# Kernel tuning notes

Hardware: AMD Instinct MI355X
Metric: run time of the kernel (lower is better)

Reference implementation:

```python
import jax, jax.numpy as jnp
import numpy as np
import math

B, S, H = 2, 2048, 1024
NH = 16
HD = H // NH  # 64


def setup_inputs() -> dict:
    key = jax.random.key(0)
    ks = jax.random.split(key, 4)
    scale = 1.0 / math.sqrt(H)
    return {
        "hidden_states": jax.random.normal(ks[0], (B, S, H), dtype=jnp.float32),
        "attention_mask": jnp.ones((B, S), dtype=jnp.float32),
        "Wq": jax.random.normal(ks[1], (H, H), dtype=jnp.float32) * scale,
        "bq": jnp.zeros((H,), dtype=jnp.float32),
        "Wk": jax.random.normal(ks[2], (H, H), dtype=jnp.float32) * scale,
        "bk": jnp.zeros((H,), dtype=jnp.float32),
        "Wv": jax.random.normal(ks[3], (H, H), dtype=jnp.float32) * scale,
        "bv": jnp.zeros((H,), dtype=jnp.float32),
    }


def _split_heads(x):
    # [B, S, H] -> [B, NH, S, HD]
    b, s, _ = x.shape
    return x.reshape(b, s, NH, HD).transpose(0, 2, 1, 3)


def reference(hidden_states, attention_mask, Wq, bq, Wk, bk, Wv, bv):
    q = _split_heads(hidden_states @ Wq.T + bq)  # [B, NH, S, HD]
    k = _split_heads(hidden_states @ Wk.T + bk)
    v = _split_heads(hidden_states @ Wv.T + bv)

    # [B, NH, S, S] attention scores
    scores = jnp.einsum("bhqd,bhkd->bhqk", q, k) / math.sqrt(HD)
    # mask: [B, S] -> additive bias [B, 1, 1, S]
    bias = (1.0 - attention_mask)[:, None, None, :] * -10000.0
    probs = jax.nn.softmax(scores + bias, axis=-1)
    # dropout prob = 0.0 (eval semantics) -> identity

    ctx = jnp.einsum("bhqk,bhkd->bhqd", probs, v)  # [B, NH, S, HD]
    ctx = ctx.transpose(0, 2, 1, 3).reshape(hidden_states.shape[0], hidden_states.shape[1], H)
    return ctx
```

## Files before the change

kernel.cpp:

```cpp
#include <hip/hip_runtime.h>
#include <hip/hip_bf16.h>

typedef __bf16 bf16;
typedef __bf16 bf16x4 __attribute__((ext_vector_type(4)));
typedef __bf16 bf16x8 __attribute__((ext_vector_type(8)));
typedef float f32x4 __attribute__((ext_vector_type(4)));

#define GLP(p) ((const __attribute__((address_space(1))) void*)(p))
#define LDSP(p) ((__attribute__((address_space(3))) void*)(p))

__global__ __launch_bounds__(256) void cvt_kernel(const float* __restrict__ in,
                                                  bf16* __restrict__ out, int n4) {
  int i = blockIdx.x * 256 + threadIdx.x;
  if (i < n4) {
    float4 v = reinterpret_cast<const float4*>(in)[i];
    bf16x4 o = { (bf16)v.x, (bf16)v.y, (bf16)v.z, (bf16)v.w };
    reinterpret_cast<bf16x4*>(out)[i] = o;
  }
}

__global__ __launch_bounds__(256) void qkv_gemm(
    const bf16* __restrict__ Xb, const bf16* __restrict__ Wb,
    const float* __restrict__ biasq, const float* __restrict__ biask,
    const float* __restrict__ biasv,
    bf16* __restrict__ Qb, bf16* __restrict__ Kb, bf16* __restrict__ Vt) {
  __shared__ __align__(16) bf16 As[128 * 32];
  __shared__ __align__(16) bf16 Bs[128 * 32];
  const int tid = threadIdx.x;
  const int w = tid >> 6, l = tid & 63;
  const int lg = l >> 4, lr = l & 15;
  const int wr = w >> 1, wc = w & 1;
  const int bm = blockIdx.y * 128, bn = blockIdx.x * 128;

  f32x4 acc[4][4] = {};

  #pragma unroll 1
  for (int k0 = 0; k0 < 1024; k0 += 32) {
    #pragma unroll
    for (int i = 0; i < 2; ++i) {
      int row = i * 64 + (tid >> 2);
      int c8 = (tid & 3) * 8;
      __builtin_amdgcn_global_load_lds(GLP(Xb + (bm + row) * 1024 + k0 + c8),
                                       LDSP((char*)As + (i * 256 + w * 64) * 16),
                                       16, 0, 0);
      __builtin_amdgcn_global_load_lds(GLP(Wb + (bn + row) * 1024 + k0 + c8),
                                       LDSP((char*)Bs + (i * 256 + w * 64) * 16),
                                       16, 0, 0);
    }
    __syncthreads();
    bf16x8 af[4], bfq[4];
    #pragma unroll
    for (int t = 0; t < 4; ++t) {
      af[t]  = *reinterpret_cast<const bf16x8*>(
                   reinterpret_cast<const char*>(As) + (wr * 64 + t * 16 + lr) * 64 + lg * 16);
      bfq[t] = *reinterpret_cast<const bf16x8*>(
                   reinterpret_cast<const char*>(Bs) + (wc * 64 + t * 16 + lr) * 64 + lg * 16);
    }
    #pragma unroll
    for (int mt = 0; mt < 4; ++mt)
      #pragma unroll
      for (int nt = 0; nt < 4; ++nt)
        acc[mt][nt] = __builtin_amdgcn_mfma_f32_16x16x32_bf16(af[mt], bfq[nt], acc[mt][nt], 0, 0, 0);
    __syncthreads();
  }

  const int mtx = blockIdx.x >> 3;
  const float* bp = (mtx == 0) ? biasq : (mtx == 1) ? biask : biasv;
  #pragma unroll
  for (int nt = 0; nt < 4; ++nt) {
    int ng = bn + wc * 64 + nt * 16 + lr;
    int nj = ng & 1023;
    int hh = nj >> 6, d = nj & 63;
    float bias = bp[nj];
    #pragma unroll
    for (int mt = 0; mt < 4; ++mt) {
      int m0 = bm + wr * 64 + mt * 16 + lg * 4;
      int bb = m0 >> 11, s0 = m0 & 2047;
      if (mtx == 2) {
        bf16x4 pk;
        #pragma unroll
        for (int r = 0; r < 4; ++r) pk[r] = (bf16)(acc[mt][nt][r] + bias);
        *reinterpret_cast<bf16x4*>(Vt + (((bb * 16 + hh) * 64 + d) * 2048 + s0)) = pk;
      } else {
        bf16* dst = (mtx == 0) ? Qb : Kb;
        #pragma unroll
        for (int r = 0; r < 4; ++r)
          dst[((bb * 16 + hh) * 2048 + s0 + r) * 64 + d] = (bf16)(acc[mt][nt][r] + bias);
      }
    }
  }
}

__global__ __launch_bounds__(256) void attn_kernel(
    const bf16* __restrict__ Qb, const bf16* __restrict__ Kb,
    const bf16* __restrict__ Vt, const float* __restrict__ mask,
    float* __restrict__ out) {
  __shared__ __align__(16) bf16 Ks[64 * 64];
  __shared__ __align__(16) bf16 Vs[64 * 64];
  __shared__ __align__(16) bf16 Pl[4][16 * 72];
  const int tid = threadIdx.x;
  const int w = tid >> 6, l = tid & 63;
  const int lg = l >> 4, lr = l & 15;
  const int blk = blockIdx.x;
  const int xcd = blk & 7, i0 = blk >> 3;
  const int bh = xcd * 4 + (i0 >> 5), qt = i0 & 31;
  const int bb = bh >> 4, hh = bh & 15;
  const int q16 = qt * 64 + w * 16;

  const bf16* Qp = Qb + (bh * 2048 + q16) * 64;
  const bf16* Kp = Kb + bh * 2048 * 64;
  const bf16* Vp = Vt + bh * 64 * 2048;
  const float* mp = mask + bb * 2048;

  bf16x8 aq[2];
  #pragma unroll
  for (int kk = 0; kk < 2; ++kk)
    aq[kk] = *reinterpret_cast<const bf16x8*>(Qp + lr * 64 + kk * 32 + lg * 8);

  f32x4 acc[4] = {};
  float mrun = -3.0e38f;
  float lrun = 0.f;

  const float SC = 0.125f * 1.44269504f;
  const float MB = -10000.0f * 1.44269504f;
  bf16* pw = &Pl[w][0];
  const int srow = tid >> 3, sch = tid & 7;

  #pragma unroll 1
  for (int kv0 = 0; kv0 < 2048; kv0 += 64) {
    #pragma unroll
    for (int p = 0; p < 2; ++p) {
      int rw = p * 32 + srow;
      int chg = sch ^ (rw & 7);
      __builtin_amdgcn_global_load_lds(GLP(Kp + (kv0 + rw) * 64 + chg * 8),
                                       LDSP((char*)Ks + (p * 256 + w * 64) * 16), 16, 0, 0);
      __builtin_amdgcn_global_load_lds(GLP(Vp + rw * 2048 + kv0 + chg * 8),
                                       LDSP((char*)Vs + (p * 256 + w * 64) * 16), 16, 0, 0);
    }
    __syncthreads();

    f32x4 sa[4];
    #pragma unroll
    for (int t = 0; t < 4; ++t) {
      f32x4 z = {};
      #pragma unroll
      for (int kk = 0; kk < 2; ++kk) {
        bf16x8 bk8 = *reinterpret_cast<const bf16x8*>(
            reinterpret_cast<const char*>(Ks) + (t * 16 + lr) * 128 + ((kk * 4 + lg) ^ (lr & 7)) * 16);
        z = __builtin_amdgcn_mfma_f32_16x16x32_bf16(bk8, aq[kk], z, 0, 0, 0);
      }
      sa[t] = z;
    }
    #pragma unroll
    for (int t = 0; t < 4; ++t) {
      float4 mk = *reinterpret_cast<const float4*>(mp + kv0 + t * 16 + lg * 4);
      sa[t][0] = sa[t][0] * SC + (1.0f - mk.x) * MB;
      sa[t][1] = sa[t][1] * SC + (1.0f - mk.y) * MB;
      sa[t][2] = sa[t][2] * SC + (1.0f - mk.z) * MB;
      sa[t][3] = sa[t][3] * SC + (1.0f - mk.w) * MB;
    }
    float rm = sa[0][0];
    #pragma unroll
    for (int t = 0; t < 4; ++t)
      #pragma unroll
      for (int r = 0; r < 4; ++r) rm = fmaxf(rm, sa[t][r]);
    rm = fmaxf(rm, __shfl_xor(rm, 16));
    rm = fmaxf(rm, __shfl_xor(rm, 32));
    float mn = fmaxf(mrun, rm);
    float fac = exp2f(mrun - mn);
    mrun = mn;
    float rs = 0.f;
    #pragma unroll
    for (int t = 0; t < 4; ++t)
      #pragma unroll
      for (int r = 0; r < 4; ++r) {
        float p = exp2f(sa[t][r] - mn);
        sa[t][r] = p;
        rs += p;
      }
    rs += __shfl_xor(rs, 16);
    rs += __shfl_xor(rs, 32);
    lrun = lrun * fac + rs;
    float facq[4];
    #pragma unroll
    for (int r = 0; r < 4; ++r) facq[r] = __shfl(fac, ((l >> 4) << 2) + r);
    #pragma unroll
    for (int nt = 0; nt < 4; ++nt)
      #pragma unroll
      for (int r = 0; r < 4; ++r) acc[nt][r] *= facq[r];
    #pragma unroll
    for (int t = 0; t < 4; ++t) {
      bf16x4 pk = { (bf16)sa[t][0], (bf16)sa[t][1], (bf16)sa[t][2], (bf16)sa[t][3] };
      *reinterpret_cast<bf16x4*>(pw + lr * 72 + t * 16 + lg * 4) = pk;
    }
    asm volatile("" ::: "memory");
    #pragma unroll
    for (int ks = 0; ks < 2; ++ks) {
      bf16x8 pa = *reinterpret_cast<const bf16x8*>(
          reinterpret_cast<const char*>(pw) + lr * 144 + ks * 64 + lg * 16);
      #pragma unroll
      for (int nt = 0; nt < 4; ++nt) {
        bf16x8 bv8 = *reinterpret_cast<const bf16x8*>(
            reinterpret_cast<const char*>(Vs) + (nt * 16 + lr) * 128 + ((ks * 4 + lg) ^ (lr & 7)) * 16);
        acc[nt] = __builtin_amdgcn_mfma_f32_16x16x32_bf16(pa, bv8, acc[nt], 0, 0, 0);
      }
    }
    __syncthreads();
  }

  #pragma unroll
  for (int r = 0; r < 4; ++r) {
    float lq = __shfl(lrun, ((l >> 4) << 2) + r);
    float inv = 1.0f / lq;
    int sq = q16 + lg * 4 + r;
    #pragma unroll
    for (int nt = 0; nt < 4; ++nt) {
      int d = nt * 16 + lr;
      out[((bb * 2048 + sq) * 16 + hh) * 64 + d] = acc[nt][r] * inv;
    }
  }
}

extern "C" void kernel_launch(void* const* d_in, const int* in_sizes, int n_in,
                              void* d_out, int out_size, void* d_ws, size_t ws_size,
                              hipStream_t stream) {
  const float* hs   = (const float*)d_in[0];
  const float* mask = (const float*)d_in[1];
  const float* Wq   = (const float*)d_in[2];
  const float* bq   = (const float*)d_in[3];
  const float* Wk   = (const float*)d_in[4];
  const float* bk   = (const float*)d_in[5];
  const float* Wv   = (const float*)d_in[6];
  const float* bv   = (const float*)d_in[7];
  float* out = (float*)d_out;

  if (ws_size < 39845888u) return;
  bf16* Xb = (bf16*)d_ws;
  bf16* Wb = Xb + 4194304;
  bf16* Qb = Wb + 3145728;
  bf16* Kb = Qb + 4194304;
  bf16* Vt = Kb + 4194304;

  cvt_kernel<<<4096, 256, 0, stream>>>(hs, Xb, 1048576);
  cvt_kernel<<<1024, 256, 0, stream>>>(Wq, Wb, 262144);
  cvt_kernel<<<1024, 256, 0, stream>>>(Wk, Wb + 1048576, 262144);
  cvt_kernel<<<1024, 256, 0, stream>>>(Wv, Wb + 2097152, 262144);
  qkv_gemm<<<dim3(24, 32), 256, 0, stream>>>(Xb, Wb, bq, bk, bv, Qb, Kb, Vt);
  attn_kernel<<<1024, 256, 0, stream>>>(Qb, Kb, Vt, mask, out);
}
```

Before: 219.8 us.

## Fuse conversions, fold softmax scale into Q, skip all-ones mask and lazy rescale

Merges the four fp32-to-bf16 conversion launches into one kernel. The softmax scale and log2(e) factor are folded into Q in the projection epilogue, so the attention loop no longer multiplies scores by them. Each wave scans the mask once and skips per-tile mask loads when every entry is 1. It also rescales the running accumulator only when the row max grows by more than 8 (a lazy online-softmax threshold) and computes the row max as a tree. The lazy rescale lets exp2 arguments reach up to 2^8, and the mask skip is a data-dependent fast path.

```diff
diff --git a/kernel.cpp b/kernel.cpp
--- a/kernel.cpp
+++ b/kernel.cpp
@@ -9,14 +9,26 @@
 #define GLP(p) ((const __attribute__((address_space(1))) void*)(p))
 #define LDSP(p) ((__attribute__((address_space(3))) void*)(p))
 
-__global__ __launch_bounds__(256) void cvt_kernel(const float* __restrict__ in,
-                                                  bf16* __restrict__ out, int n4) {
+__global__ __launch_bounds__(256) void cvt_all_kernel(
+    const float* __restrict__ hs, const float* __restrict__ Wq,
+    const float* __restrict__ Wk, const float* __restrict__ Wv,
+    bf16* __restrict__ Xb, bf16* __restrict__ Wb) {
   int i = blockIdx.x * 256 + threadIdx.x;
-  if (i < n4) {
-    float4 v = reinterpret_cast<const float4*>(in)[i];
-    bf16x4 o = { (bf16)v.x, (bf16)v.y, (bf16)v.z, (bf16)v.w };
-    reinterpret_cast<bf16x4*>(out)[i] = o;
-  }
+  const float* src;
+  bf16* dst;
+  int off;
+  if (i < 1048576) {
+    src = hs; dst = Xb; off = i;
+  } else {
+    int j = i - 1048576;
+    int which = j >> 18;
+    off = j & 262143;
+    src = (which == 0) ? Wq : (which == 1) ? Wk : Wv;
+    dst = Wb + (which << 20);
+  }
+  float4 v = *reinterpret_cast<const float4*>(src + off * 4);
+  bf16x4 o = { (bf16)v.x, (bf16)v.y, (bf16)v.z, (bf16)v.w };
+  *reinterpret_cast<bf16x4*>(dst + off * 4) = o;
 }
 
 __global__ __launch_bounds__(256) void qkv_gemm(
@@ -66,6 +78,7 @@
 
   const int mtx = blockIdx.x >> 3;
   const float* bp = (mtx == 0) ? biasq : (mtx == 1) ? biask : biasv;
+  const float scale = (mtx == 0) ? 0.18033688f : 1.0f;
   #pragma unroll
   for (int nt = 0; nt < 4; ++nt) {
     int ng = bn + wc * 64 + nt * 16 + lr;
@@ -85,7 +98,7 @@
         bf16* dst = (mtx == 0) ? Qb : Kb;
         #pragma unroll
         for (int r = 0; r < 4; ++r)
-          dst[((bb * 16 + hh) * 2048 + s0 + r) * 64 + d] = (bf16)(acc[mt][nt][r] + bias);
+          dst[((bb * 16 + hh) * 2048 + s0 + r) * 64 + d] = (bf16)((acc[mt][nt][r] + bias) * scale);
       }
     }
   }
@@ -112,6 +125,14 @@
   const bf16* Vp = Vt + bh * 64 * 2048;
   const float* mp = mask + bb * 2048;
 
+  bool nm = false;
+  #pragma unroll
+  for (int i = 0; i < 8; ++i) {
+    float4 mv = *reinterpret_cast<const float4*>(mp + i * 256 + l * 4);
+    nm |= (mv.x != 1.f) | (mv.y != 1.f) | (mv.z != 1.f) | (mv.w != 1.f);
+  }
+  const bool need_mask = __any(nm);
+
   bf16x8 aq[2];
   #pragma unroll
   for (int kk = 0; kk < 2; ++kk)
@@ -121,7 +142,6 @@
   float mrun = -3.0e38f;
   float lrun = 0.f;
 
-  const float SC = 0.125f * 1.44269504f;
   const float MB = -10000.0f * 1.44269504f;
   bf16* pw = &Pl[w][0];
   const int srow = tid >> 3, sch = tid & 7;
@@ -151,43 +171,49 @@
       }
       sa[t] = z;
     }
-    #pragma unroll
-    for (int t = 0; t < 4; ++t) {
-      float4 mk = *reinterpret_cast<const float4*>(mp + kv0 + t * 16 + lg * 4);
-      sa[t][0] = sa[t][0] * SC + (1.0f - mk.x) * MB;
-      sa[t][1] = sa[t][1] * SC + (1.0f - mk.y) * MB;
-      sa[t][2] = sa[t][2] * SC + (1.0f - mk.z) * MB;
-      sa[t][3] = sa[t][3] * SC + (1.0f - mk.w) * MB;
-    }
-    float rm = sa[0][0];
-    #pragma unroll
-    for (int t = 0; t < 4; ++t)
-      #pragma unroll
-      for (int r = 0; r < 4; ++r) rm = fmaxf(rm, sa[t][r]);
+    if (need_mask) {
+      #pragma unroll
+      for (int t = 0; t < 4; ++t) {
+        float4 mk = *reinterpret_cast<const float4*>(mp + kv0 + t * 16 + lg * 4);
+        sa[t][0] += (1.0f - mk.x) * MB;
+        sa[t][1] += (1.0f - mk.y) * MB;
+        sa[t][2] += (1.0f - mk.z) * MB;
+        sa[t][3] += (1.0f - mk.w) * MB;
+      }
+    }
+    f32x4 mx01 = { fmaxf(sa[0][0], sa[1][0]), fmaxf(sa[0][1], sa[1][1]),
+                   fmaxf(sa[0][2], sa[1][2]), fmaxf(sa[0][3], sa[1][3]) };
+    f32x4 mx23 = { fmaxf(sa[2][0], sa[3][0]), fmaxf(sa[2][1], sa[3][1]),
+                   fmaxf(sa[2][2], sa[3][2]), fmaxf(sa[2][3], sa[3][3]) };
+    float rm = fmaxf(fmaxf(fmaxf(mx01[0], mx23[0]), fmaxf(mx01[1], mx23[1])),
+                     fmaxf(fmaxf(mx01[2], mx23[2]), fmaxf(mx01[3], mx23[3])));
     rm = fmaxf(rm, __shfl_xor(rm, 16));
     rm = fmaxf(rm, __shfl_xor(rm, 32));
-    float mn = fmaxf(mrun, rm);
-    float fac = exp2f(mrun - mn);
-    mrun = mn;
+    if (__any(rm > mrun + 8.f)) {
+      float mn = fmaxf(mrun, rm);
+      float fac = exp2f(mrun - mn);
+      mrun = mn;
+      lrun *= fac;
+      float facq[4];
+      #pragma unroll
+      for (int r = 0; r < 4; ++r) facq[r] = __shfl(fac, ((l >> 4) << 2) + r);
+      #pragma unroll
+      for (int nt = 0; nt < 4; ++nt)
+        #pragma unroll
+        for (int r = 0; r < 4; ++r) acc[nt][r] *= facq[r];
+    }
     float rs = 0.f;
     #pragma unroll
     for (int t = 0; t < 4; ++t)
       #pragma unroll
       for (int r = 0; r < 4; ++r) {
-        float p = exp2f(sa[t][r] - mn);
+        float p = exp2f(sa[t][r] - mrun);
         sa[t][r] = p;
         rs += p;
       }
     rs += __shfl_xor(rs, 16);
     rs += __shfl_xor(rs, 32);
-    lrun = lrun * fac + rs;
-    float facq[4];
-    #pragma unroll
-    for (int r = 0; r < 4; ++r) facq[r] = __shfl(fac, ((l >> 4) << 2) + r);
-    #pragma unroll
-    for (int nt = 0; nt < 4; ++nt)
-      #pragma unroll
-      for (int r = 0; r < 4; ++r) acc[nt][r] *= facq[r];
+    lrun += rs;
     #pragma unroll
     for (int t = 0; t < 4; ++t) {
       bf16x4 pk = { (bf16)sa[t][0], (bf16)sa[t][1], (bf16)sa[t][2], (bf16)sa[t][3] };
@@ -241,10 +267,7 @@
   bf16* Kb = Qb + 4194304;
   bf16* Vt = Kb + 4194304;
 
-  cvt_kernel<<<4096, 256, 0, stream>>>(hs, Xb, 1048576);
-  cvt_kernel<<<1024, 256, 0, stream>>>(Wq, Wb, 262144);
-  cvt_kernel<<<1024, 256, 0, stream>>>(Wk, Wb + 1048576, 262144);
-  cvt_kernel<<<1024, 256, 0, stream>>>(Wv, Wb + 2097152, 262144);
+  cvt_all_kernel<<<7168, 256, 0, stream>>>(hs, Wq, Wk, Wv, Xb, Wb);
   qkv_gemm<<<dim3(24, 32), 256, 0, stream>>>(Xb, Wb, bq, bk, bv, Qb, Kb, Vt);
   attn_kernel<<<1024, 256, 0, stream>>>(Qb, Kb, Vt, mask, out);
 }
```

Measured after the change: 201.4 us. -8.4%, faster.
